# Kernel optimization log

Hardware: AMD Instinct MI355X
Metric: run time of the kernel (lower is better)

Reference implementation:

```python
import jax, jax.numpy as jnp
import numpy as np
from jax import lax

# --- model/problem dims (see init_kwargs) ---
G, NPG, R, F, HID, L = 40, 500, 8, 256, 256, 3   # graphs(frames), nodes/graph, relations, feat, hidden, layers
N = G * NPG                                       # 20000 nodes
EPG = 8000
E = G * EPG                                       # 320000 edges
TOTAL = L * HID                                   # 768 = concat of layer outputs
LSTM_IN, LSTM_HID, NCLASS = 256, 256, 2
RATIO = 0.5
K = int(np.ceil(RATIO * NPG))                     # 250 nodes kept per graph by SAGPool


def setup_inputs() -> dict:
    key = jax.random.key(0)
    ks = jax.random.split(key, 16)
    s = 0.05
    x = jax.random.normal(ks[0], (N, F), dtype=jnp.float32)
    # intra-graph edges: node ids offset by graph index
    off = jnp.arange(G, dtype=jnp.int32)[:, None] * NPG
    src = jax.random.randint(ks[1], (G, EPG), 0, NPG, dtype=jnp.int32) + off
    dst = jax.random.randint(ks[2], (G, EPG), 0, NPG, dtype=jnp.int32) + off
    edge_index = jnp.stack([src.reshape(-1), dst.reshape(-1)])
    edge_attr = jax.random.randint(ks[3], (E,), 0, R, dtype=jnp.int32)
    batch = jnp.repeat(jnp.arange(G, dtype=jnp.int32), NPG)
    # RGCN layer params (layer0 in=F==HID so all layers stack)
    conv_W = jax.random.normal(ks[4], (L, R, HID, HID), dtype=jnp.float32) * s
    conv_root = jax.random.normal(ks[5], (L, HID, HID), dtype=jnp.float32) * s
    conv_bias = jnp.zeros((L, HID), dtype=jnp.float32)
    # SAGPool scorer: RGCNConv(TOTAL, 1, R)
    pool_W = jax.random.normal(ks[6], (R, TOTAL, 1), dtype=jnp.float32) * s
    pool_root = jax.random.normal(ks[7], (TOTAL, 1), dtype=jnp.float32) * s
    pool_bias = jnp.zeros((1,), dtype=jnp.float32)
    fc1_W = jax.random.normal(ks[8], (LSTM_IN, TOTAL), dtype=jnp.float32) * s
    fc1_b = jnp.zeros((LSTM_IN,), dtype=jnp.float32)
    W_ih = jax.random.normal(ks[9], (4 * LSTM_HID, LSTM_IN), dtype=jnp.float32) * s
    W_hh = jax.random.normal(ks[10], (4 * LSTM_HID, LSTM_HID), dtype=jnp.float32) * s
    b_ih = jnp.zeros((4 * LSTM_HID,), dtype=jnp.float32)
    b_hh = jnp.zeros((4 * LSTM_HID,), dtype=jnp.float32)
    fc2_W = jax.random.normal(ks[11], (NCLASS, LSTM_HID), dtype=jnp.float32) * s
    fc2_b = jnp.zeros((NCLASS,), dtype=jnp.float32)
    return dict(x=x, edge_index=edge_index, edge_attr=edge_attr, batch=batch,
                conv_W=conv_W, conv_root=conv_root, conv_bias=conv_bias,
                pool_W=pool_W, pool_root=pool_root, pool_bias=pool_bias,
                fc1_W=fc1_W, fc1_b=fc1_b, W_ih=W_ih, W_hh=W_hh, b_ih=b_ih, b_hh=b_hh,
                fc2_W=fc2_W, fc2_b=fc2_b)


def rgcn_conv(x, src, dst, etype, W, root, bias):
    """PyG (Fast)RGCNConv: per-relation mean aggregation summed over relations + root + bias."""
    num_nodes = x.shape[0]
    Rr = W.shape[0]
    h_all = jnp.einsum('ni,rio->rno', x, W)          # [R, N, out] per-relation transform
    msg = h_all[etype, src]                           # [E, out] per-edge message
    seg = dst * Rr + etype                            # (node, relation) segment id
    cnt = jax.ops.segment_sum(jnp.ones((src.shape[0],), x.dtype), seg,
                              num_segments=num_nodes * Rr)
    norm = 1.0 / jnp.maximum(cnt[seg], 1.0)           # per-(dst,rel) mean normalization
    agg = jax.ops.segment_sum(msg * norm[:, None], dst, num_segments=num_nodes)
    return agg + x @ root + bias


def lstm_scan(xs, W_ih, W_hh, b_ih, b_hh):
    """torch.nn.LSTM (single layer, batch=1) over sequence xs [T, in]; torch gate order i,f,g,o."""
    H = W_hh.shape[1]
    def step(carry, xt):
        h, c = carry
        gates = xt @ W_ih.T + h @ W_hh.T + b_ih + b_hh
        i, f, g, o = jnp.split(gates, 4)
        c = jax.nn.sigmoid(f) * c + jax.nn.sigmoid(i) * jnp.tanh(g)
        h = jax.nn.sigmoid(o) * jnp.tanh(c)
        return (h, c), h
    init = (jnp.zeros((H,), xs.dtype), jnp.zeros((H,), xs.dtype))
    (h, c), ys = lax.scan(step, init, xs)
    return ys, h


def reference(x, edge_index, edge_attr, batch,
              conv_W, conv_root, conv_bias,
              pool_W, pool_root, pool_bias,
              fc1_W, fc1_b, W_ih, W_hh, b_ih, b_hh, fc2_W, fc2_b):
    src, dst = edge_index[0], edge_index[1]
    # stacked RGCN layers, outputs concatenated (dropout omitted: eval mode)
    h = x
    outs = []
    for l in range(L):
        h = jax.nn.relu(rgcn_conv(h, src, dst, edge_attr, conv_W[l], conv_root[l], conv_bias[l]))
        outs.append(h)
    xc = jnp.concatenate(outs, axis=-1)               # [N, TOTAL]
    # SAGPool: RGCN scorer -> tanh -> per-graph top-k (batch is contiguous equal-size graphs)
    score = jnp.tanh(rgcn_conv(xc, src, dst, edge_attr, pool_W, pool_root, pool_bias).reshape(-1))
    topv, topi = lax.top_k(score.reshape(G, NPG), K)  # [G, K]
    xg = xc.reshape(G, NPG, TOTAL)
    xsel = jnp.take_along_axis(xg, topi[:, :, None], axis=1) * topv[:, :, None]
    # readout_type='mean': global_mean_pool over kept nodes per graph
    readout = xsel.mean(axis=1)                       # [G, TOTAL]
    h1 = jax.nn.relu(readout @ fc1_W.T + fc1_b)       # [G, LSTM_IN]
    # temporal_type='lstm_last': last hidden state over the G-frame sequence
    _, hlast = lstm_scan(h1, W_ih, W_hh, b_ih, b_hh)  # [LSTM_HID]
    logits = hlast @ fc2_W.T + fc2_b                  # [NCLASS]
    return jax.nn.log_softmax(logits, axis=-1)
```

## Files before the change

### kernel.cpp

```cpp
#include <hip/hip_runtime.h>

typedef unsigned short u16;
typedef short bf8 __attribute__((ext_vector_type(8)));
typedef float f4 __attribute__((ext_vector_type(4)));
typedef _Float16 h2v __attribute__((ext_vector_type(2)));
typedef __fp16 g2v __attribute__((ext_vector_type(2)));

#define N_NODES 20000
#define N_EDGES 320000
#define NGRAPH 40
#define NPG 500
#define KTOP 250
#define NSEG (N_NODES * 8)
#define NM (N_NODES * 256)

#define P_CONV_BIAS 0
#define P_POOL_W    768
#define P_POOL_ROOT 6912
#define P_POOL_BIAS 7680
#define P_FC1_W     7688
#define P_FC1_B     204296
#define P_W_IH      204552
#define P_B_IH      466696
#define P_B_HH      467720
#define P_FC2_W     468744
#define P_FC2_B     469256
#define P_TOTAL     469264

__device__ __forceinline__ float b2f(u16 u) {
    union { unsigned int i; float f; } v; v.i = ((unsigned int)u) << 16; return v.f;
}
__device__ __forceinline__ u16 f2b(float f) {
    union { float f; unsigned int i; } v; v.f = f;
    unsigned int x = v.i;
    return (u16)((x + 0x7fffu + ((x >> 16) & 1u)) >> 16);
}
__device__ __forceinline__ float wred(float s) {
    #pragma unroll
    for (int off = 32; off > 0; off >>= 1) s += __shfl_down(s, off);
    return s;
}
__device__ __forceinline__ float fdot2u(unsigned a, unsigned b, float c) {
#if __has_builtin(__builtin_amdgcn_fdot2)
    union { unsigned u; h2v h; } ua, ub; ua.u = a; ub.u = b;
    return __builtin_amdgcn_fdot2(ua.h, ub.h, c, false);
#else
    union { unsigned u; g2v h; } ua, ub; ua.u = a; ub.u = b;
    return c + (float)ua.h[0] * (float)ub.h[0] + (float)ua.h[1] * (float)ub.h[1];
#endif
}
__device__ __forceinline__ unsigned packh2(float a, float b) {
    g2v h = __builtin_amdgcn_cvt_pkrtz(a, b);
    union { g2v h; unsigned u; } v; v.h = h; return v.u;
}

__global__ void k_init(unsigned int* __restrict__ flag, unsigned int* __restrict__ cnt,
                       unsigned int* __restrict__ ctr) {
    int i = blockIdx.x * 256 + threadIdx.x;
    if (i < 64) flag[i] = 0u;
    if (i < NSEG) { cnt[i] = 0u; ctr[i] = 0u; }
}

__global__ void k_detect1(const u16* __restrict__ xr, int n, unsigned int* __restrict__ fb) {
    unsigned int local = 0;
    for (int i = blockIdx.x * 256 + threadIdx.x; i < n; i += 64 * 256) {
        unsigned int u = xr[i];
        if (((u >> 7) & 0xFFu) == 0xFFu) local++;
    }
    local = (unsigned int)wred((float)local);
    if ((threadIdx.x & 63) == 0 && local) atomicAdd(&fb[1], local);
}
__global__ void k_detect2(unsigned int* __restrict__ fb) {
    fb[0] = (fb[1] > 8u) ? 1u : 0u;
}

__device__ __forceinline__ u16 load_cvt(const void* src, size_t i, bool f32) {
    return f32 ? f2b(((const float*)src)[i]) : ((const u16*)src)[i];
}

__global__ void k_cvt_all(const void* conv_bias, const void* pool_W, const void* pool_root,
                          const void* pool_bias, const void* fc1_W, const void* fc1_b,
                          const void* W_ih, const void* b_ih, const void* b_hh,
                          const void* fc2_W, const void* fc2_b,
                          u16* __restrict__ parms, const unsigned int* __restrict__ flag) {
    int i = blockIdx.x * 256 + threadIdx.x;
    if (i >= P_TOTAL) return;
    bool f32 = (*flag != 0u);
    u16 v;
    if      (i < P_CONV_BIAS + 768)    v = load_cvt(conv_bias, i - P_CONV_BIAS, f32);
    else if (i < P_POOL_W + 6144)      v = load_cvt(pool_W,    i - P_POOL_W, f32);
    else if (i < P_POOL_ROOT + 768)    v = load_cvt(pool_root, i - P_POOL_ROOT, f32);
    else if (i < P_POOL_BIAS + 1)      v = load_cvt(pool_bias, i - P_POOL_BIAS, f32);
    else if (i < P_FC1_W && i >= P_POOL_BIAS) return;
    else if (i < P_FC1_W + 196608)     v = load_cvt(fc1_W,    i - P_FC1_W, f32);
    else if (i < P_FC1_B + 256)        v = load_cvt(fc1_b,    i - P_FC1_B, f32);
    else if (i < P_W_IH + 262144)      v = load_cvt(W_ih,     i - P_W_IH, f32);
    else if (i < P_B_IH + 1024)        v = load_cvt(b_ih,     i - P_B_IH, f32);
    else if (i < P_B_HH + 1024)        v = load_cvt(b_hh,     i - P_B_HH, f32);
    else if (i < P_FC2_W + 512)        v = load_cvt(fc2_W,    i - P_FC2_W, f32);
    else if (i < P_FC2_B + 2)          v = load_cvt(fc2_b,    i - P_FC2_B, f32);
    else return;
    parms[i] = v;
}

__global__ void k_stage_x(const void* __restrict__ src, u16* __restrict__ xc,
                          const unsigned int* __restrict__ flag) {
    int i = blockIdx.x * 256 + threadIdx.x;
    if (i >= N_NODES * 256) return;
    u16 v = load_cvt(src, i, *flag != 0u);
    int n = i >> 8, f = i & 255;
    xc[(size_t)n * 768 + 512 + f] = v;
}

__global__ void k_count(const int* __restrict__ dst, const int* __restrict__ et,
                        unsigned int* __restrict__ cnt) {
    int e = blockIdx.x * 256 + threadIdx.x;
    if (e < N_EDGES) {
        unsigned d = (unsigned)dst[e]; if (d >= N_NODES) d = 0;
        unsigned r = (unsigned)et[e] & 7u;
        atomicAdd(&cnt[d * 8 + r], 1u);
    }
}
__global__ void k_inv(const unsigned int* __restrict__ cnt, float* __restrict__ inv, int n) {
    int i = blockIdx.x * 256 + threadIdx.x;
    if (i < n) {
        unsigned int c = cnt[i];
        inv[i] = 1.0f / (float)(c < 1u ? 1u : c);
    }
}

__global__ void k_scan1(const unsigned int* __restrict__ cnt, unsigned int* __restrict__ seg,
                        unsigned int* __restrict__ bsum) {
    __shared__ unsigned int s[256];
    int t = threadIdx.x, i = blockIdx.x * 256 + t;
    unsigned int v = (i < NSEG) ? cnt[i] : 0u;
    s[t] = v;
    __syncthreads();
    for (int off = 1; off < 256; off <<= 1) {
        unsigned int add = (t >= off) ? s[t - off] : 0u;
        __syncthreads();
        s[t] += add;
        __syncthreads();
    }
    if (i < NSEG) seg[i] = s[t] - v;
    if (t == 255) bsum[blockIdx.x] = s[255];
}
__global__ void k_scan2(unsigned int* __restrict__ bsum, int nb) {
    __shared__ unsigned int s[1024];
    int t = threadIdx.x;
    unsigned int v = (t < nb) ? bsum[t] : 0u;
    s[t] = v;
    __syncthreads();
    for (int off = 1; off < 1024; off <<= 1) {
        unsigned int add = (t >= off) ? s[t - off] : 0u;
        __syncthreads();
        s[t] += add;
        __syncthreads();
    }
    if (t < nb) bsum[t] = s[t] - v;
}
__global__ void k_scan3(unsigned int* __restrict__ seg, const unsigned int* __restrict__ bsum) {
    int i = blockIdx.x * 256 + threadIdx.x;
    if (i < NSEG) seg[i] += bsum[i >> 8];
    if (i == 0) seg[NSEG] = N_EDGES;
}
__global__ void k_place(const int* __restrict__ src, const int* __restrict__ dst,
                        const int* __restrict__ et, const unsigned int* __restrict__ seg,
                        unsigned int* __restrict__ ctr, const float* __restrict__ inv,
                        unsigned int* __restrict__ skey, float* __restrict__ sw) {
    int e = blockIdx.x * 256 + threadIdx.x;
    if (e >= N_EDGES) return;
    unsigned s = (unsigned)src[e]; if (s >= N_NODES) s = 0;
    unsigned d = (unsigned)dst[e]; if (d >= N_NODES) d = 0;
    unsigned r = (unsigned)et[e] & 7u;
    unsigned key = d * 8 + r;
    unsigned pos = seg[key] + atomicAdd(&ctr[key], 1u);
    skey[pos] = s;
    sw[pos] = inv[key];
}

__global__ void k_transpose2(const void* __restrict__ conv_W, const void* __restrict__ conv_root,
                             u16* __restrict__ Wt, const unsigned int* __restrict__ flag) {
    int idx = blockIdx.x * 256 + threadIdx.x;
    if (idx >= 3 * 256 * 2304) return;
    bool f32 = (*flag != 0u);
    int k = idx % 2304;
    int o = (idx / 2304) % 256;
    int l = idx / (2304 * 256);
    u16 v;
    if (k < 2048) {
        int r = k >> 8, i = k & 255;
        v = load_cvt(conv_W, ((size_t)((l * 8 + r) * 256 + i)) * 256 + o, f32);
    } else {
        int i = k - 2048;
        v = load_cvt(conv_root, ((size_t)(l * 256 + i)) * 256 + o, f32);
    }
    Wt[idx] = v;
}
__global__ void k_whh2(const void* __restrict__ W_hh, unsigned int* __restrict__ whh2,
                       const unsigned int* __restrict__ flag) {
    int idx = blockIdx.x * 256 + threadIdx.x;
    if (idx >= 128 * 1024) return;
    int i2 = idx >> 10, j = idx & 1023;
    bool f32 = (*flag != 0u);
    float a, b;
    if (f32) {
        a = ((const float*)W_hh)[j * 256 + 2 * i2];
        b = ((const float*)W_hh)[j * 256 + 2 * i2 + 1];
    } else {
        a = b2f(((const u16*)W_hh)[j * 256 + 2 * i2]);
        b = b2f(((const u16*)W_hh)[j * 256 + 2 * i2 + 1]);
    }
    whh2[idx] = packh2(a, b);
}

__launch_bounds__(256)
__global__ void k_gather_y(const unsigned int* __restrict__ seg,
                           const unsigned int* __restrict__ skey,
                           const float* __restrict__ sw,
                           const u16* __restrict__ xprev,
                           u16* __restrict__ Y, int r0, int RC) {
    int d = blockIdx.x, f = threadIdx.x;
    for (int rr = 0; rr < RC; ++rr) {
        int r = r0 + rr;
        unsigned nb = seg[d * 8 + r], ne = seg[d * 8 + r + 1];
        float acc = 0.0f;
        for (unsigned i = nb; i < ne; ++i)
            acc += sw[i] * b2f(xprev[(size_t)skey[i] * 768 + f]);
        Y[((size_t)d * RC + rr) * 256 + f] = f2b(acc);
    }
}

template<int EPI, int INCR>
__launch_bounds__(256)
__global__ void k_gemm2(const u16* __restrict__ Y, int strideY, int KY,
                        const u16* __restrict__ xroot, const u16* __restrict__ Bt,
                        int kbase, const u16* __restrict__ bias,
                        float* __restrict__ agg, u16* __restrict__ xc, int colbase) {
    __shared__ u16 lb[128 * 72];
    int n0 = blockIdx.x * 128;
    int wave = threadIdx.x >> 6, lane = threadIdx.x & 63;
    int m0 = blockIdx.y * 64 + wave * 16;
    int mrow = lane & 15, quad = lane >> 4;
    int mclamp = m0 + mrow; if (mclamp > N_NODES - 1) mclamp = N_NODES - 1;

    f4 acc[8];
    #pragma unroll
    for (int nt = 0; nt < 8; ++nt) acc[nt] = (f4){0.0f, 0.0f, 0.0f, 0.0f};

    int cy = KY >> 6;
    int nchunks = cy + (INCR ? 4 : 0);
    int brow = threadIdx.x >> 1;
    int bcol = (threadIdx.x & 1) * 32;
    const u16* bsrc = Bt + (size_t)(n0 + brow) * 2304 + bcol;
    u16* bdst = lb + brow * 72 + bcol;

    for (int ck = 0; ck < nchunks; ++ck) {
        bool isroot = INCR && (ck >= cy);
        int kg = isroot ? (2048 + ((ck - cy) << 6)) : (kbase + (ck << 6));
        __syncthreads();
        #pragma unroll
        for (int c = 0; c < 4; ++c)
            *(bf8*)(bdst + c * 8) = *(const bf8*)(bsrc + kg + c * 8);
        __syncthreads();
        const u16* arow = isroot ? (xroot + (size_t)mclamp * 768 + ((ck - cy) << 6))
                                 : (Y + (size_t)mclamp * strideY + (ck << 6));
        bf8 a0 = *(const bf8*)(arow + quad * 8);
        bf8 a1 = *(const bf8*)(arow + quad * 8 + 32);
        #pragma unroll
        for (int nt = 0; nt < 8; ++nt) {
            const u16* lbp = lb + (nt * 16 + mrow) * 72 + quad * 8;
            bf8 b0 = *(const bf8*)(lbp);
            bf8 b1 = *(const bf8*)(lbp + 32);
            acc[nt] = __builtin_amdgcn_mfma_f32_16x16x32_bf16(a0, b0, acc[nt], 0, 0, 0);
            acc[nt] = __builtin_amdgcn_mfma_f32_16x16x32_bf16(a1, b1, acc[nt], 0, 0, 0);
        }
    }

    if (EPI == 0) {
        __syncthreads();
        u16* tb = lb + wave * 2176;
        #pragma unroll
        for (int nt = 0; nt < 8; ++nt)
            #pragma unroll
            for (int v = 0; v < 4; ++v) {
                int o = n0 + nt * 16 + mrow;
                float val = acc[nt][v] + b2f(bias[o]);
                val = val > 0.0f ? val : 0.0f;
                tb[(quad * 4 + v) * 136 + nt * 16 + mrow] = f2b(val);
            }
        __syncthreads();
        int srow = lane >> 2, scol = (lane & 3) * 32;
        int m = m0 + srow;
        if (m < N_NODES) {
            u16* dst = xc + (size_t)m * 768 + colbase + n0 + scol;
            const u16* srcp = tb + srow * 136 + scol;
            #pragma unroll
            for (int c = 0; c < 4; ++c)
                *(bf8*)(dst + c * 8) = *(const bf8*)(srcp + c * 8);
        }
    } else {
        #pragma unroll
        for (int nt = 0; nt < 8; ++nt)
            #pragma unroll
            for (int v = 0; v < 4; ++v) {
                int m = m0 + quad * 4 + v;
                if (m >= N_NODES) continue;
                int o = n0 + nt * 16 + mrow;
                if (EPI == 1) {
                    agg[(size_t)m * 256 + o] = acc[nt][v] + b2f(bias[o]);
                } else if (EPI == 2) {
                    agg[(size_t)m * 256 + o] += acc[nt][v];
                } else {
                    float s = agg[(size_t)m * 256 + o] + acc[nt][v];
                    s = s > 0.0f ? s : 0.0f;
                    xc[(size_t)m * 768 + colbase + o] = f2b(s);
                }
            }
    }
}

__launch_bounds__(256)
__global__ void k_pool(const u16* __restrict__ xc, const u16* __restrict__ parms,
                       float* __restrict__ p, float* __restrict__ score) {
    int n = blockIdx.x * 4 + (threadIdx.x >> 6);
    if (n >= N_NODES) return;
    int lane = threadIdx.x & 63;
    const u16* xr = xc + (size_t)n * 768;
    float acc[9];
    #pragma unroll
    for (int rr = 0; rr < 9; ++rr) acc[rr] = 0.0f;
    #pragma unroll
    for (int q = 0; q < 12; ++q) {
        int f = lane + 64 * q;
        float xv = b2f(xr[f]);
        #pragma unroll
        for (int rr = 0; rr < 8; ++rr)
            acc[rr] += xv * b2f(parms[P_POOL_W + rr * 768 + f]);
        acc[8] += xv * b2f(parms[P_POOL_ROOT + f]);
    }
    #pragma unroll
    for (int rr = 0; rr < 9; ++rr) acc[rr] = wred(acc[rr]);
    if (lane == 0) {
        #pragma unroll
        for (int rr = 0; rr < 8; ++rr) p[rr * N_NODES + n] = acc[rr];
        score[n] = acc[8] + b2f(parms[P_POOL_BIAS]);
    }
}
__global__ void k_scatter_pool(const int* __restrict__ src, const int* __restrict__ dst,
                               const int* __restrict__ et, const float* __restrict__ inv,
                               const float* __restrict__ p, float* __restrict__ score) {
    int e = blockIdx.x * 256 + threadIdx.x;
    if (e >= N_EDGES) return;
    int r = et[e] & 7;
    unsigned s = (unsigned)src[e]; if (s >= N_NODES) s = 0;
    unsigned d = (unsigned)dst[e]; if (d >= N_NODES) d = 0;
    atomicAdd(&score[d], inv[d * 8 + r] * p[r * N_NODES + s]);
}

__launch_bounds__(256)
__global__ void k_sort(const float* __restrict__ score, unsigned int* __restrict__ topidx,
                       float* __restrict__ topv) {
    __shared__ unsigned long long keys[512];
    __shared__ float vals[512];
    int g = blockIdx.x, tid = threadIdx.x;
    for (int i = tid; i < 512; i += 256) {
        unsigned long long key;
        float v = 0.0f;
        if (i < NPG) {
            v = tanhf(score[g * NPG + i]);
            unsigned int u = __float_as_uint(v);
            u = (u & 0x80000000u) ? ~u : (u | 0x80000000u);
            u = ~u;
            key = ((unsigned long long)u << 32) | (unsigned int)i;
        } else {
            key = 0xFFFFFFFFFFFFFFFFull;
        }
        keys[i] = key;
        vals[i] = v;
    }
    __syncthreads();
    for (int k = 2; k <= 512; k <<= 1)
        for (int j = k >> 1; j > 0; j >>= 1) {
            for (int i = tid; i < 512; i += 256) {
                int ixj = i ^ j;
                if (ixj > i) {
                    bool up = ((i & k) == 0);
                    unsigned long long a = keys[i], b = keys[ixj];
                    if ((a > b) == up) { keys[i] = b; keys[ixj] = a; }
                }
            }
            __syncthreads();
        }
    if (tid < KTOP) {
        int idx = (int)(keys[tid] & 511u);
        topidx[g * 256 + tid] = (unsigned)idx;
        topv[g * 256 + tid] = vals[idx];
    }
}

__launch_bounds__(256)
__global__ void k_readout(const unsigned int* __restrict__ topidx,
                          const float* __restrict__ topv,
                          const u16* __restrict__ xc, float* __restrict__ readout) {
    __shared__ unsigned int sidx[KTOP];
    __shared__ float sv[KTOP];
    __shared__ float part[256];
    int g = blockIdx.x, cb = blockIdx.y;
    int tid = threadIdx.x;
    if (tid < KTOP) { sidx[tid] = topidx[g * 256 + tid]; sv[tid] = topv[g * 256 + tid]; }
    __syncthreads();
    int fl = tid & 63, ng = tid >> 6;
    int f = cb * 64 + fl;
    float acc = 0.0f;
    for (int j = ng; j < KTOP; j += 4)
        acc += sv[j] * b2f(xc[(size_t)(g * NPG + sidx[j]) * 768 + f]);
    part[tid] = acc;
    __syncthreads();
    if (tid < 64) {
        float s = part[tid] + part[64 + tid] + part[128 + tid] + part[192 + tid];
        readout[(size_t)g * 768 + cb * 64 + tid] = s * (1.0f / (float)KTOP);
    }
}

__global__ void k_fc1(const float* __restrict__ readout, const u16* __restrict__ parms,
                      float* __restrict__ h1) {
    int wid = blockIdx.x * 4 + (threadIdx.x >> 6);
    if (wid >= NGRAPH * 256) return;
    int g = wid >> 8, o = wid & 255, lane = threadIdx.x & 63;
    const float* rr = readout + (size_t)g * 768;
    const u16* w = parms + P_FC1_W + (size_t)o * 768;
    float s = 0.0f;
    #pragma unroll
    for (int q = 0; q < 12; ++q) { int f = lane + 64 * q; s += rr[f] * b2f(w[f]); }
    s = wred(s);
    if (lane == 0) { s += b2f(parms[P_FC1_B + o]); h1[g * 256 + o] = s > 0.0f ? s : 0.0f; }
}
__global__ void k_gx(const float* __restrict__ h1, const u16* __restrict__ parms,
                     float* __restrict__ gx) {
    int wid = blockIdx.x * 4 + (threadIdx.x >> 6);
    if (wid >= NGRAPH * 1024) return;
    int t = wid >> 10, j = wid & 1023, lane = threadIdx.x & 63;
    const float* xr = h1 + t * 256;
    const u16* w = parms + P_W_IH + (size_t)j * 256;
    float s = 0.0f;
    #pragma unroll
    for (int q = 0; q < 4; ++q) { int f = lane + 64 * q; s += xr[f] * b2f(w[f]); }
    s = wred(s);
    if (lane == 0) gx[t * 1024 + j] = s + b2f(parms[P_B_IH + j]) + b2f(parms[P_B_HH + j]);
}

__launch_bounds__(1024, 4)
__global__ void k_lstm(const float* __restrict__ gx, const unsigned int* __restrict__ whh2,
                       const u16* __restrict__ parms, void* __restrict__ out,
                       const unsigned int* __restrict__ flag) {
    __shared__ float hs[256];
    __shared__ unsigned int hs2[128];
    __shared__ float gs[1024];
    __shared__ float red[2];
    int tid = threadIdx.x;
    unsigned int wreg[64];
    #pragma unroll
    for (int i = 0; i < 64; ++i) wreg[i] = whh2[i * 1024 + tid];
    if (tid < 256) hs[tid] = 0.0f;
    if (tid < 128) hs2[tid] = 0u;
    float c = 0.0f;
    __syncthreads();
    for (int t = 0; t < NGRAPH; ++t) {
        float g = gx[t * 1024 + tid];
        #pragma unroll
        for (int i = 0; i < 64; ++i) g = fdot2u(wreg[i], hs2[i], g);
        #pragma unroll 8
        for (int i = 64; i < 128; ++i) g = fdot2u(whh2[i * 1024 + tid], hs2[i], g);
        gs[tid] = g;
        __syncthreads();
        if (tid < 256) {
            float gi = 1.0f / (1.0f + expf(-gs[tid]));
            float gf = 1.0f / (1.0f + expf(-gs[256 + tid]));
            float gg = tanhf(gs[512 + tid]);
            float go = 1.0f / (1.0f + expf(-gs[768 + tid]));
            c = gf * c + gi * gg;
            float h = go * tanhf(c);
            hs[tid] = h;
            float ho = __shfl(h, (tid & 63) ^ 1);
            if (!(tid & 1)) hs2[tid >> 1] = packh2(h, ho);
        }
        __syncthreads();
    }
    if (tid < 128) {
        int cls = tid >> 6, lane = tid & 63;
        float s = 0.0f;
        #pragma unroll
        for (int q = 0; q < 4; ++q) {
            int d = lane + 64 * q;
            s += hs[d] * b2f(parms[P_FC2_W + cls * 256 + d]);
        }
        s = wred(s);
        if (lane == 0) red[cls] = s + b2f(parms[P_FC2_B + cls]);
    }
    __syncthreads();
    if (tid == 0) {
        float l0 = red[0], l1 = red[1];
        float m = fmaxf(l0, l1);
        float lse = m + logf(expf(l0 - m) + expf(l1 - m));
        float o0 = l0 - lse, o1 = l1 - lse;
        if (*flag) { ((float*)out)[0] = o0; ((float*)out)[1] = o1; }
        else       { ((u16*)out)[0] = f2b(o0); ((u16*)out)[1] = f2b(o1); }
    }
}

struct WS {
    unsigned int* flag; unsigned int* cnt; float* inv; unsigned int* seg; unsigned int* ctr;
    unsigned int* skey; float* sw; unsigned int* bsum;
    u16* Wt2; u16* Y; float* agg; u16* xc; float* p; float* score;
    unsigned int* topidx; float* topv;
    float* readout; float* h1; float* gx; unsigned int* whh2; u16* parms;
    size_t need;
};
static WS plan(char* base, int RC) {
    WS w; size_t off = 0;
    auto take = [&](size_t bytes) -> char* {
        char* p = base + off; off += (bytes + 255) & ~(size_t)255; return p;
    };
    w.flag    = (unsigned int*)take(256);
    w.cnt     = (unsigned int*)take((size_t)NSEG * 4);
    w.inv     = (float*)take((size_t)NSEG * 4);
    w.seg     = (unsigned int*)take((size_t)(NSEG + 1) * 4);
    w.ctr     = (unsigned int*)take((size_t)NSEG * 4);
    w.skey    = (unsigned int*)take((size_t)N_EDGES * 4);
    w.sw      = (float*)take((size_t)N_EDGES * 4);
    w.bsum    = (unsigned int*)take(1024 * 4);
    w.Wt2     = (u16*)take((size_t)3 * 256 * 2304 * 2);
    w.Y       = (u16*)take((size_t)N_NODES * RC * 256 * 2);
    w.agg     = (RC < 8) ? (float*)take((size_t)NM * 4) : nullptr;
    w.xc      = (u16*)take((size_t)N_NODES * 768 * 2);
    w.p       = (float*)take((size_t)8 * N_NODES * 4);
    w.score   = (float*)take((size_t)N_NODES * 4);
    w.topidx  = (unsigned int*)take((size_t)NGRAPH * 256 * 4);
    w.topv    = (float*)take((size_t)NGRAPH * 256 * 4);
    w.readout = (float*)take((size_t)NGRAPH * 768 * 4);
    w.h1      = (float*)take((size_t)NGRAPH * 256 * 4);
    w.gx      = (float*)take((size_t)NGRAPH * 1024 * 4);
    w.whh2    = (unsigned int*)take((size_t)128 * 1024 * 4);
    w.parms   = (u16*)take((size_t)P_TOTAL * 2);
    w.need = off;
    return w;
}

static void run_layers2(const WS& w, int RC, hipStream_t stream) {
    const dim3 ggrid(2, 313);
    const int npass = 8 / RC;
    const int KY = RC * 256;
    for (int l = 0; l < 3; ++l) {
        const u16* xprev = w.xc + (l == 0 ? 512 : (l - 1) * 256);
        const u16* Bt = w.Wt2 + (size_t)l * 2304 * 256;
        const u16* bias = w.parms + P_CONV_BIAS + l * 256;
        for (int p = 0; p < npass; ++p) {
            k_gather_y<<<N_NODES, 256, 0, stream>>>(w.seg, w.skey, w.sw, xprev,
                                                    w.Y, p * RC, RC);
            int kbase = p * RC * 256;
            if (npass == 1)
                k_gemm2<0, 1><<<ggrid, 256, 0, stream>>>(w.Y, KY, KY, xprev, Bt, kbase,
                                                         bias, w.agg, w.xc, l * 256);
            else if (p == 0)
                k_gemm2<1, 1><<<ggrid, 256, 0, stream>>>(w.Y, KY, KY, xprev, Bt, kbase,
                                                         bias, w.agg, w.xc, l * 256);
            else if (p == npass - 1)
                k_gemm2<3, 0><<<ggrid, 256, 0, stream>>>(w.Y, KY, KY, xprev, Bt, kbase,
                                                         bias, w.agg, w.xc, l * 256);
            else
                k_gemm2<2, 0><<<ggrid, 256, 0, stream>>>(w.Y, KY, KY, xprev, Bt, kbase,
                                                         bias, w.agg, w.xc, l * 256);
        }
    }
}

extern "C" void kernel_launch(void* const* d_in, const int* in_sizes, int n_in,
                              void* d_out, int out_size, void* d_ws, size_t ws_size,
                              hipStream_t stream) {
    (void)in_sizes; (void)n_in; (void)out_size;
    const void* x        = d_in[0];
    const int* edge_index= (const int*)d_in[1];
    const int* edge_attr = (const int*)d_in[2];
    const void* conv_W   = d_in[4];
    const void* conv_root= d_in[5];
    const void* conv_bias= d_in[6];
    const void* pool_W   = d_in[7];
    const void* pool_root= d_in[8];
    const void* pool_bias= d_in[9];
    const void* fc1_W    = d_in[10];
    const void* fc1_b    = d_in[11];
    const void* W_ih     = d_in[12];
    const void* W_hh     = d_in[13];
    const void* b_ih     = d_in[14];
    const void* b_hh     = d_in[15];
    const void* fc2_W    = d_in[16];
    const void* fc2_b    = d_in[17];

    const int* e_src = edge_index;
    const int* e_dst = edge_index + N_EDGES;

    int RC = 1;
    if (plan((char*)d_ws, 8).need <= ws_size)      RC = 8;
    else if (plan((char*)d_ws, 4).need <= ws_size) RC = 4;
    else if (plan((char*)d_ws, 2).need <= ws_size) RC = 2;
    WS w = plan((char*)d_ws, RC);

    k_init<<<(NSEG + 255) / 256, 256, 0, stream>>>(w.flag, w.cnt, w.ctr);
    k_detect1<<<64, 256, 0, stream>>>((const u16*)x, 1 << 20, w.flag);
    k_detect2<<<1, 1, 0, stream>>>(w.flag);

    k_count<<<1250, 256, 0, stream>>>(e_dst, edge_attr, w.cnt);
    k_inv<<<(NSEG + 255) / 256, 256, 0, stream>>>(w.cnt, w.inv, NSEG);
    k_scan1<<<625, 256, 0, stream>>>(w.cnt, w.seg, w.bsum);
    k_scan2<<<1, 1024, 0, stream>>>(w.bsum, 625);
    k_scan3<<<(NSEG + 255) / 256, 256, 0, stream>>>(w.seg, w.bsum);
    k_place<<<1250, 256, 0, stream>>>(e_src, e_dst, edge_attr, w.seg, w.ctr, w.inv,
                                      w.skey, w.sw);

    k_cvt_all<<<(P_TOTAL + 255) / 256, 256, 0, stream>>>(
        conv_bias, pool_W, pool_root, pool_bias, fc1_W, fc1_b,
        W_ih, b_ih, b_hh, fc2_W, fc2_b, w.parms, w.flag);

    k_stage_x<<<20000, 256, 0, stream>>>(x, w.xc, w.flag);
    k_transpose2<<<6912, 256, 0, stream>>>(conv_W, conv_root, w.Wt2, w.flag);
    k_whh2<<<512, 256, 0, stream>>>(W_hh, w.whh2, w.flag);

    run_layers2(w, RC, stream);

    k_pool<<<5000, 256, 0, stream>>>(w.xc, w.parms, w.p, w.score);
    k_scatter_pool<<<1250, 256, 0, stream>>>(e_src, e_dst, edge_attr, w.inv, w.p, w.score);
    k_sort<<<NGRAPH, 256, 0, stream>>>(w.score, w.topidx, w.topv);
    k_readout<<<dim3(NGRAPH, 12), 256, 0, stream>>>(w.topidx, w.topv, w.xc, w.readout);
    k_fc1<<<2560, 256, 0, stream>>>(w.readout, w.parms, w.h1);
    k_gx<<<10240, 256, 0, stream>>>(w.h1, w.parms, w.gx);
    k_lstm<<<1, 1024, 0, stream>>>(w.gx, w.whh2, w.parms, d_out, w.flag);
}
```

Baseline: 794.3 us.

## Fuse RGCN neighbor gather and GEMM into one per-layer kernel

Replaces the separate gather-to-Y and GEMM passes per layer with a single kernel. For each 32-node tile, the kernel gathers the per-relation neighbor sums into shared memory and immediately feeds them to MFMA against a pre-chunked weight layout. This removes the large Y/agg intermediate buffers, their global memory traffic and the multi-pass launches. In exchange, each block recomputes its gathers serially with fewer nodes per tile, and the weights are reloaded once per block. It also vectorises the LSTM W_hh register loads to 128-bit and shrinks the dtype-detect scan.

Result: slower. 1.011 ms (+27.3%).

```diff
diff --git a/kernel.cpp b/kernel.cpp
--- a/kernel.cpp
+++ b/kernel.cpp
@@ -5,6 +5,7 @@
 typedef float f4 __attribute__((ext_vector_type(4)));
 typedef _Float16 h2v __attribute__((ext_vector_type(2)));
 typedef __fp16 g2v __attribute__((ext_vector_type(2)));
+typedef unsigned int u4v __attribute__((ext_vector_type(4)));
 
 #define N_NODES 20000
 #define N_EDGES 320000
@@ -12,7 +13,6 @@
 #define NPG 500
 #define KTOP 250
 #define NSEG (N_NODES * 8)
-#define NM (N_NODES * 256)
 
 #define P_CONV_BIAS 0
 #define P_POOL_W    768
@@ -182,26 +182,29 @@
 __global__ void k_transpose2(const void* __restrict__ conv_W, const void* __restrict__ conv_root,
                              u16* __restrict__ Wt, const unsigned int* __restrict__ flag) {
     int idx = blockIdx.x * 256 + threadIdx.x;
-    if (idx >= 3 * 256 * 2304) return;
+    if (idx >= 3 * 36 * 256 * 64) return;
     bool f32 = (*flag != 0u);
-    int k = idx % 2304;
-    int o = (idx / 2304) % 256;
-    int l = idx / (2304 * 256);
+    int kk = idx & 63;
+    int n = (idx >> 6) & 255;
+    int lc = idx >> 14;
+    int l = lc / 36, ck = lc % 36;
+    int k = ck * 64 + kk;
     u16 v;
     if (k < 2048) {
         int r = k >> 8, i = k & 255;
-        v = load_cvt(conv_W, ((size_t)((l * 8 + r) * 256 + i)) * 256 + o, f32);
+        v = load_cvt(conv_W, ((size_t)((l * 8 + r) * 256 + i)) * 256 + n, f32);
     } else {
         int i = k - 2048;
-        v = load_cvt(conv_root, ((size_t)(l * 256 + i)) * 256 + o, f32);
+        v = load_cvt(conv_root, ((size_t)(l * 256 + i)) * 256 + n, f32);
     }
     Wt[idx] = v;
 }
-__global__ void k_whh2(const void* __restrict__ W_hh, unsigned int* __restrict__ whh2,
+__global__ void k_whh4(const void* __restrict__ W_hh, unsigned int* __restrict__ whh4,
                        const unsigned int* __restrict__ flag) {
     int idx = blockIdx.x * 256 + threadIdx.x;
-    if (idx >= 128 * 1024) return;
-    int i2 = idx >> 10, j = idx & 1023;
+    if (idx >= 32 * 1024 * 4) return;
+    int c = idx & 3, j = (idx >> 2) & 1023, i4 = idx >> 12;
+    int i2 = i4 * 4 + c;
     bool f32 = (*flag != 0u);
     float a, b;
     if (f32) {
@@ -211,113 +214,94 @@
         a = b2f(((const u16*)W_hh)[j * 256 + 2 * i2]);
         b = b2f(((const u16*)W_hh)[j * 256 + 2 * i2 + 1]);
     }
-    whh2[idx] = packh2(a, b);
-}
-
-__launch_bounds__(256)
-__global__ void k_gather_y(const unsigned int* __restrict__ seg,
-                           const unsigned int* __restrict__ skey,
-                           const float* __restrict__ sw,
-                           const u16* __restrict__ xprev,
-                           u16* __restrict__ Y, int r0, int RC) {
-    int d = blockIdx.x, f = threadIdx.x;
-    for (int rr = 0; rr < RC; ++rr) {
-        int r = r0 + rr;
-        unsigned nb = seg[d * 8 + r], ne = seg[d * 8 + r + 1];
-        float acc = 0.0f;
-        for (unsigned i = nb; i < ne; ++i)
-            acc += sw[i] * b2f(xprev[(size_t)skey[i] * 768 + f]);
-        Y[((size_t)d * RC + rr) * 256 + f] = f2b(acc);
-    }
-}
-
-template<int EPI, int INCR>
-__launch_bounds__(256)
-__global__ void k_gemm2(const u16* __restrict__ Y, int strideY, int KY,
-                        const u16* __restrict__ xroot, const u16* __restrict__ Bt,
-                        int kbase, const u16* __restrict__ bias,
-                        float* __restrict__ agg, u16* __restrict__ xc, int colbase) {
-    __shared__ u16 lb[128 * 72];
-    int n0 = blockIdx.x * 128;
+    whh4[idx] = packh2(a, b);
+}
+
+__launch_bounds__(256, 2)
+__global__ void k_layer(const unsigned int* __restrict__ seg,
+                        const unsigned int* __restrict__ skey,
+                        const float* __restrict__ sw,
+                        const u16* __restrict__ xprev,
+                        const u16* __restrict__ WtL,
+                        const u16* __restrict__ bias,
+                        u16* __restrict__ xc, int colbase) {
+    __shared__ u16 As[32 * 264];
+    __shared__ u16 Bs[256 * 72];
     int wave = threadIdx.x >> 6, lane = threadIdx.x & 63;
-    int m0 = blockIdx.y * 64 + wave * 16;
+    int m0 = blockIdx.x * 32;
     int mrow = lane & 15, quad = lane >> 4;
-    int mclamp = m0 + mrow; if (mclamp > N_NODES - 1) mclamp = N_NODES - 1;
+    int arow = (wave & 1) * 16 + mrow;
+    int nbase = (wave >> 1) * 128;
 
     f4 acc[8];
     #pragma unroll
     for (int nt = 0; nt < 8; ++nt) acc[nt] = (f4){0.0f, 0.0f, 0.0f, 0.0f};
 
-    int cy = KY >> 6;
-    int nchunks = cy + (INCR ? 4 : 0);
-    int brow = threadIdx.x >> 1;
-    int bcol = (threadIdx.x & 1) * 32;
-    const u16* bsrc = Bt + (size_t)(n0 + brow) * 2304 + bcol;
-    u16* bdst = lb + brow * 72 + bcol;
-
-    for (int ck = 0; ck < nchunks; ++ck) {
-        bool isroot = INCR && (ck >= cy);
-        int kg = isroot ? (2048 + ((ck - cy) << 6)) : (kbase + (ck << 6));
+    for (int rg = 0; rg < 9; ++rg) {
         __syncthreads();
+        #pragma unroll 2
+        for (int j = 0; j < 8; ++j) {
+            int row = wave * 8 + j;
+            int m = m0 + row;
+            ushort4 o;
+            if (rg < 8) {
+                unsigned nb = seg[m * 8 + rg], ne = seg[m * 8 + rg + 1];
+                float a0 = 0.0f, a1 = 0.0f, a2 = 0.0f, a3 = 0.0f;
+                for (unsigned i = nb; i < ne; ++i) {
+                    float wgt = sw[i];
+                    ushort4 u = *(const ushort4*)(xprev + (size_t)skey[i] * 768 + lane * 4);
+                    a0 += wgt * b2f(u.x); a1 += wgt * b2f(u.y);
+                    a2 += wgt * b2f(u.z); a3 += wgt * b2f(u.w);
+                }
+                o.x = f2b(a0); o.y = f2b(a1); o.z = f2b(a2); o.w = f2b(a3);
+            } else {
+                o = *(const ushort4*)(xprev + (size_t)m * 768 + lane * 4);
+            }
+            *(ushort4*)(As + row * 264 + lane * 4) = o;
+        }
         #pragma unroll
-        for (int c = 0; c < 4; ++c)
-            *(bf8*)(bdst + c * 8) = *(const bf8*)(bsrc + kg + c * 8);
-        __syncthreads();
-        const u16* arow = isroot ? (xroot + (size_t)mclamp * 768 + ((ck - cy) << 6))
-                                 : (Y + (size_t)mclamp * strideY + (ck << 6));
-        bf8 a0 = *(const bf8*)(arow + quad * 8);
-        bf8 a1 = *(const bf8*)(arow + quad * 8 + 32);
-        #pragma unroll
-        for (int nt = 0; nt < 8; ++nt) {
-            const u16* lbp = lb + (nt * 16 + mrow) * 72 + quad * 8;
-            bf8 b0 = *(const bf8*)(lbp);
-            bf8 b1 = *(const bf8*)(lbp + 32);
-            acc[nt] = __builtin_amdgcn_mfma_f32_16x16x32_bf16(a0, b0, acc[nt], 0, 0, 0);
-            acc[nt] = __builtin_amdgcn_mfma_f32_16x16x32_bf16(a1, b1, acc[nt], 0, 0, 0);
-        }
-    }
-
-    if (EPI == 0) {
-        __syncthreads();
-        u16* tb = lb + wave * 2176;
-        #pragma unroll
-        for (int nt = 0; nt < 8; ++nt)
+        for (int c4 = 0; c4 < 4; ++c4) {
+            int ck = rg * 4 + c4;
+            __syncthreads();
+            {
+                const u16* srcp = WtL + (size_t)ck * 16384 + threadIdx.x * 64;
+                u16* dstp = Bs + threadIdx.x * 72;
+                #pragma unroll
+                for (int c = 0; c < 8; ++c)
+                    *(bf8*)(dstp + c * 8) = *(const bf8*)(srcp + c * 8);
+            }
+            __syncthreads();
             #pragma unroll
-            for (int v = 0; v < 4; ++v) {
-                int o = n0 + nt * 16 + mrow;
-                float val = acc[nt][v] + b2f(bias[o]);
-                val = val > 0.0f ? val : 0.0f;
-                tb[(quad * 4 + v) * 136 + nt * 16 + mrow] = f2b(val);
-            }
-        __syncthreads();
-        int srow = lane >> 2, scol = (lane & 3) * 32;
-        int m = m0 + srow;
-        if (m < N_NODES) {
-            u16* dst = xc + (size_t)m * 768 + colbase + n0 + scol;
-            const u16* srcp = tb + srow * 136 + scol;
-            #pragma unroll
-            for (int c = 0; c < 4; ++c)
-                *(bf8*)(dst + c * 8) = *(const bf8*)(srcp + c * 8);
-        }
-    } else {
-        #pragma unroll
-        for (int nt = 0; nt < 8; ++nt)
-            #pragma unroll
-            for (int v = 0; v < 4; ++v) {
-                int m = m0 + quad * 4 + v;
-                if (m >= N_NODES) continue;
-                int o = n0 + nt * 16 + mrow;
-                if (EPI == 1) {
-                    agg[(size_t)m * 256 + o] = acc[nt][v] + b2f(bias[o]);
-                } else if (EPI == 2) {
-                    agg[(size_t)m * 256 + o] += acc[nt][v];
-                } else {
-                    float s = agg[(size_t)m * 256 + o] + acc[nt][v];
-                    s = s > 0.0f ? s : 0.0f;
-                    xc[(size_t)m * 768 + colbase + o] = f2b(s);
+            for (int ks = 0; ks < 2; ++ks) {
+                bf8 a = *(const bf8*)(As + arow * 264 + c4 * 64 + ks * 32 + quad * 8);
+                #pragma unroll
+                for (int nt = 0; nt < 8; ++nt) {
+                    bf8 b = *(const bf8*)(Bs + (nbase + nt * 16 + mrow) * 72 + ks * 32 + quad * 8);
+                    acc[nt] = __builtin_amdgcn_mfma_f32_16x16x32_bf16(a, b, acc[nt], 0, 0, 0);
                 }
             }
-    }
+        }
+    }
+    __syncthreads();
+    #pragma unroll
+    for (int nt = 0; nt < 8; ++nt) {
+        int col = nbase + nt * 16 + mrow;
+        float bv = b2f(bias[col]);
+        #pragma unroll
+        for (int v = 0; v < 4; ++v) {
+            float val = acc[nt][v] + bv;
+            val = val > 0.0f ? val : 0.0f;
+            As[((wave & 1) * 16 + quad * 4 + v) * 264 + col] = f2b(val);
+        }
+    }
+    __syncthreads();
+    int row = threadIdx.x >> 3;
+    int c0 = (threadIdx.x & 7) * 32;
+    u16* dst = xc + (size_t)(m0 + row) * 768 + colbase + c0;
+    const u16* srcp = As + row * 264 + c0;
+    #pragma unroll
+    for (int c = 0; c < 4; ++c)
+        *(bf8*)(dst + c * 8) = *(const bf8*)(srcp + c * 8);
 }
 
 __launch_bounds__(256)
@@ -451,7 +435,7 @@
 }
 
 __launch_bounds__(1024, 4)
-__global__ void k_lstm(const float* __restrict__ gx, const unsigned int* __restrict__ whh2,
+__global__ void k_lstm(const float* __restrict__ gx, const unsigned int* __restrict__ whh4,
                        const u16* __restrict__ parms, void* __restrict__ out,
                        const unsigned int* __restrict__ flag) {
     __shared__ float hs[256];
@@ -459,9 +443,14 @@
     __shared__ float gs[1024];
     __shared__ float red[2];
     int tid = threadIdx.x;
-    unsigned int wreg[64];
-    #pragma unroll
-    for (int i = 0; i < 64; ++i) wreg[i] = whh2[i * 1024 + tid];
+    u4v wr[16];
+    #pragma unroll
+    for (int q = 0; q < 16; ++q)
+        wr[q] = *(const u4v*)(whh4 + (((size_t)q * 1024) + tid) * 4);
+    asm volatile("" : "+v"(wr[0]), "+v"(wr[1]), "+v"(wr[2]), "+v"(wr[3]),
+                      "+v"(wr[4]), "+v"(wr[5]), "+v"(wr[6]), "+v"(wr[7]),
+                      "+v"(wr[8]), "+v"(wr[9]), "+v"(wr[10]), "+v"(wr[11]),
+                      "+v"(wr[12]), "+v"(wr[13]), "+v"(wr[14]), "+v"(wr[15]));
     if (tid < 256) hs[tid] = 0.0f;
     if (tid < 128) hs2[tid] = 0u;
     float c = 0.0f;
@@ -469,9 +458,20 @@
     for (int t = 0; t < NGRAPH; ++t) {
         float g = gx[t * 1024 + tid];
         #pragma unroll
-        for (int i = 0; i < 64; ++i) g = fdot2u(wreg[i], hs2[i], g);
-        #pragma unroll 8
-        for (int i = 64; i < 128; ++i) g = fdot2u(whh2[i * 1024 + tid], hs2[i], g);
+        for (int q = 0; q < 16; ++q) {
+            g = fdot2u(wr[q][0], hs2[q * 4 + 0], g);
+            g = fdot2u(wr[q][1], hs2[q * 4 + 1], g);
+            g = fdot2u(wr[q][2], hs2[q * 4 + 2], g);
+            g = fdot2u(wr[q][3], hs2[q * 4 + 3], g);
+        }
+        #pragma unroll 4
+        for (int q = 16; q < 32; ++q) {
+            u4v wv = *(const u4v*)(whh4 + (((size_t)q * 1024) + tid) * 4);
+            g = fdot2u(wv[0], hs2[q * 4 + 0], g);
+            g = fdot2u(wv[1], hs2[q * 4 + 1], g);
+            g = fdot2u(wv[2], hs2[q * 4 + 2], g);
+            g = fdot2u(wv[3], hs2[q * 4 + 3], g);
+        }
         gs[tid] = g;
         __syncthreads();
         if (tid < 256) {
@@ -512,12 +512,12 @@
 struct WS {
     unsigned int* flag; unsigned int* cnt; float* inv; unsigned int* seg; unsigned int* ctr;
     unsigned int* skey; float* sw; unsigned int* bsum;
-    u16* Wt2; u16* Y; float* agg; u16* xc; float* p; float* score;
+    u16* Wt2; u16* xc; float* p; float* score;
     unsigned int* topidx; float* topv;
-    float* readout; float* h1; float* gx; unsigned int* whh2; u16* parms;
+    float* readout; float* h1; float* gx; unsigned int* whh4; u16* parms;
     size_t need;
 };
-static WS plan(char* base, int RC) {
+static WS plan(char* base) {
     WS w; size_t off = 0;
     auto take = [&](size_t bytes) -> char* {
         char* p = base + off; off += (bytes + 255) & ~(size_t)255; return p;
@@ -530,9 +530,7 @@
     w.skey    = (unsigned int*)take((size_t)N_EDGES * 4);
     w.sw      = (float*)take((size_t)N_EDGES * 4);
     w.bsum    = (unsigned int*)take(1024 * 4);
-    w.Wt2     = (u16*)take((size_t)3 * 256 * 2304 * 2);
-    w.Y       = (u16*)take((size_t)N_NODES * RC * 256 * 2);
-    w.agg     = (RC < 8) ? (float*)take((size_t)NM * 4) : nullptr;
+    w.Wt2     = (u16*)take((size_t)3 * 36 * 256 * 64 * 2);
     w.xc      = (u16*)take((size_t)N_NODES * 768 * 2);
     w.p       = (float*)take((size_t)8 * N_NODES * 4);
     w.score   = (float*)take((size_t)N_NODES * 4);
@@ -541,44 +539,16 @@
     w.readout = (float*)take((size_t)NGRAPH * 768 * 4);
     w.h1      = (float*)take((size_t)NGRAPH * 256 * 4);
     w.gx      = (float*)take((size_t)NGRAPH * 1024 * 4);
-    w.whh2    = (unsigned int*)take((size_t)128 * 1024 * 4);
+    w.whh4    = (unsigned int*)take((size_t)32 * 1024 * 4 * 4);
     w.parms   = (u16*)take((size_t)P_TOTAL * 2);
     w.need = off;
     return w;
 }
 
-static void run_layers2(const WS& w, int RC, hipStream_t stream) {
-    const dim3 ggrid(2, 313);
-    const int npass = 8 / RC;
-    const int KY = RC * 256;
-    for (int l = 0; l < 3; ++l) {
-        const u16* xprev = w.xc + (l == 0 ? 512 : (l - 1) * 256);
-        const u16* Bt = w.Wt2 + (size_t)l * 2304 * 256;
-        const u16* bias = w.parms + P_CONV_BIAS + l * 256;
-        for (int p = 0; p < npass; ++p) {
-            k_gather_y<<<N_NODES, 256, 0, stream>>>(w.seg, w.skey, w.sw, xprev,
-                                                    w.Y, p * RC, RC);
-            int kbase = p * RC * 256;
-            if (npass == 1)
-                k_gemm2<0, 1><<<ggrid, 256, 0, stream>>>(w.Y, KY, KY, xprev, Bt, kbase,
-                                                         bias, w.agg, w.xc, l * 256);
-            else if (p == 0)
-                k_gemm2<1, 1><<<ggrid, 256, 0, stream>>>(w.Y, KY, KY, xprev, Bt, kbase,
-                                                         bias, w.agg, w.xc, l * 256);
-            else if (p == npass - 1)
-                k_gemm2<3, 0><<<ggrid, 256, 0, stream>>>(w.Y, KY, KY, xprev, Bt, kbase,
-                                                         bias, w.agg, w.xc, l * 256);
-            else
-                k_gemm2<2, 0><<<ggrid, 256, 0, stream>>>(w.Y, KY, KY, xprev, Bt, kbase,
-                                                         bias, w.agg, w.xc, l * 256);
-        }
-    }
-}
-
 extern "C" void kernel_launch(void* const* d_in, const int* in_sizes, int n_in,
                               void* d_out, int out_size, void* d_ws, size_t ws_size,
                               hipStream_t stream) {
-    (void)in_sizes; (void)n_in; (void)out_size;
+    (void)in_sizes; (void)n_in; (void)out_size; (void)ws_size;
     const void* x        = d_in[0];
     const int* edge_index= (const int*)d_in[1];
     const int* edge_attr = (const int*)d_in[2];
@@ -600,14 +570,10 @@
     const int* e_src = edge_index;
     const int* e_dst = edge_index + N_EDGES;
 
-    int RC = 1;
-    if (plan((char*)d_ws, 8).need <= ws_size)      RC = 8;
-    else if (plan((char*)d_ws, 4).need <= ws_size) RC = 4;
-    else if (plan((char*)d_ws, 2).need <= ws_size) RC = 2;
-    WS w = plan((char*)d_ws, RC);
+    WS w = plan((char*)d_ws);
 
     k_init<<<(NSEG + 255) / 256, 256, 0, stream>>>(w.flag, w.cnt, w.ctr);
-    k_detect1<<<64, 256, 0, stream>>>((const u16*)x, 1 << 20, w.flag);
+    k_detect1<<<64, 256, 0, stream>>>((const u16*)x, 1 << 18, w.flag);
     k_detect2<<<1, 1, 0, stream>>>(w.flag);
 
     k_count<<<1250, 256, 0, stream>>>(e_dst, edge_attr, w.cnt);
@@ -624,9 +590,15 @@
 
     k_stage_x<<<20000, 256, 0, stream>>>(x, w.xc, w.flag);
     k_transpose2<<<6912, 256, 0, stream>>>(conv_W, conv_root, w.Wt2, w.flag);
-    k_whh2<<<512, 256, 0, stream>>>(W_hh, w.whh2, w.flag);
-
-    run_layers2(w, RC, stream);
+    k_whh4<<<512, 256, 0, stream>>>(W_hh, w.whh4, w.flag);
+
+    for (int l = 0; l < 3; ++l) {
+        const u16* xprev = w.xc + (l == 0 ? 512 : (l - 1) * 256);
+        const u16* WtL = w.Wt2 + (size_t)l * 36 * 16384;
+        const u16* bias = w.parms + P_CONV_BIAS + l * 256;
+        k_layer<<<625, 256, 0, stream>>>(w.seg, w.skey, w.sw, xprev, WtL, bias,
+                                         w.xc, l * 256);
+    }
 
     k_pool<<<5000, 256, 0, stream>>>(w.xc, w.parms, w.p, w.score);
     k_scatter_pool<<<1250, 256, 0, stream>>>(e_src, e_dst, edge_attr, w.inv, w.p, w.score);
@@ -634,5 +606,5 @@
     k_readout<<<dim3(NGRAPH, 12), 256, 0, stream>>>(w.topidx, w.topv, w.xc, w.readout);
     k_fc1<<<2560, 256, 0, stream>>>(w.readout, w.parms, w.h1);
     k_gx<<<10240, 256, 0, stream>>>(w.h1, w.parms, w.gx);
-    k_lstm<<<1, 1024, 0, stream>>>(w.gx, w.whh2, w.parms, d_out, w.flag);
-}
+    k_lstm<<<1, 1024, 0, stream>>>(w.gx, w.whh4, w.parms, d_out, w.flag);
+}
```
